# Kernel tuning notes

Hardware: AMD Instinct MI355X
Metric: run time of the kernel (lower is better)

## Reference

```python
import jax, jax.numpy as jnp
import numpy as np

B, T, D, H = 4, 2048, 1024, 16
DH = D // H  # 64


def setup_inputs() -> dict:
    key = jax.random.key(0)
    k1, k2, k3 = jax.random.split(key, 3)
    x = jax.random.normal(k1, (B, T, D), dtype=jnp.float32)
    w_qkv = jax.random.normal(k2, (D, 3 * D), dtype=jnp.float32) * (D ** -0.5)
    w_out = jax.random.normal(k3, (D, D), dtype=jnp.float32) * (D ** -0.5)
    return {"x": x, "w_qkv": w_qkv, "w_out": w_out}


def reference(x, w_qkv, w_out):
    b, t, d = x.shape
    qkv = jnp.einsum('btd,de->bte', x, w_qkv)  # [B,T,3D]
    q, k, v = jnp.split(qkv, 3, axis=-1)
    # [B,H,T,DH]
    q = q.reshape(b, t, H, DH).transpose(0, 2, 1, 3)
    k = k.reshape(b, t, H, DH).transpose(0, 2, 1, 3)
    v = v.reshape(b, t, H, DH).transpose(0, 2, 1, 3)
    logits = jnp.einsum('bhqd,bhkd->bhqk', q, k) * (1.0 / jnp.sqrt(jnp.float32(DH)))
    # causal bias: -inf strictly above the diagonal (key index > query index)
    causal = jnp.tril(jnp.ones((t, t), dtype=bool))
    logits = jnp.where(causal, logits, jnp.float32(-jnp.inf))
    scores = jax.nn.softmax(logits, axis=-1)
    y = jnp.einsum('bhqk,bhkd->bhqd', scores, v)
    y = y.transpose(0, 2, 1, 3).reshape(b, t, d)
    return jnp.einsum('btd,de->bte', y, w_out)
```

## Files before the change

kernel.cpp:

```cpp
#include <hip/hip_runtime.h>
#include <hip/hip_bf16.h>


namespace {
constexpr int kB = 4, kT = 2048, kD = 1024, kH = 16;
constexpr int kM = kB * kT;
constexpr int kNq = 3 * kD;
constexpr float kS = 0.180336880f;
}

typedef unsigned short u16;
typedef short bf16x8 __attribute__((ext_vector_type(8)));
typedef float f32x4 __attribute__((ext_vector_type(4)));

__device__ __forceinline__ u16 f2bf(float f) {
  unsigned int u = __float_as_uint(f);
  u += 0x7fffu + ((u >> 16) & 1u);
  return (u16)(u >> 16);
}
__device__ __forceinline__ unsigned int pack2(float a, float b) {
  return (unsigned int)f2bf(a) | ((unsigned int)f2bf(b) << 16);
}
__device__ __forceinline__ unsigned int cvtpk(float a, float b) {
  unsigned int r;
  asm("v_cvt_pk_bf16_f32 %0, %1, %2" : "=v"(r) : "v"(a), "v"(b));
  return r;
}

__device__ __forceinline__ void gload16(const u16* g, u16* l) {
  __builtin_amdgcn_global_load_lds(
      (const __attribute__((address_space(1))) unsigned int*)(uintptr_t)g,
      (__attribute__((address_space(3))) unsigned int*)(uintptr_t)l, 16, 0, 0);
}

__global__ __launch_bounds__(256) void cvt_bf16(const float* __restrict__ x,
                                                u16* __restrict__ xb) {
  const size_t i = ((size_t)blockIdx.x * 256 + threadIdx.x) * 8;
  const float4 v0 = *(const float4*)(x + i);
  const float4 v1 = *(const float4*)(x + i + 4);
  uint4 p;
  p.x = pack2(v0.x, v0.y);
  p.y = pack2(v0.z, v0.w);
  p.z = pack2(v1.x, v1.y);
  p.w = pack2(v1.z, v1.w);
  *(uint4*)(xb + i) = p;
}

__global__ __launch_bounds__(256) void transpose_bf(const float* __restrict__ W,
                                                    u16* __restrict__ WT,
                                                    int K, int N, int nscale) {
  __shared__ float T[32][33];
  const int tid = threadIdx.x;
  const int nb = blockIdx.x * 32, kb = blockIdx.y * 32;
  const int r = tid >> 3, c = (tid & 7) * 4;
  const float4 v = *(const float4*)&W[(size_t)(kb + r) * N + nb + c];
  T[r][c + 0] = v.x;
  T[r][c + 1] = v.y;
  T[r][c + 2] = v.z;
  T[r][c + 3] = v.w;
  __syncthreads();
  const float s = (nb + r < nscale) ? kS : 1.0f;
  uint2 p;
  p.x = pack2(T[c + 0][r] * s, T[c + 1][r] * s);
  p.y = pack2(T[c + 2][r] * s, T[c + 3][r] * s);
  *(uint2*)&WT[(size_t)(nb + r) * K + kb + c] = p;
}

template <bool F32OUT>
__global__ __launch_bounds__(512, 2) void gemm_mt(const u16* __restrict__ A,
                                                  const u16* __restrict__ BT,
                                                  void* __restrict__ Cv,
                                                  int lda, int ldc) {
  __shared__ u16 As[2][256 * 64];
  __shared__ u16 Bs[2][128 * 64];
  constexpr int NT = kD / 64;
  const int tid = threadIdx.x;
  const int wid = tid >> 6, lane = tid & 63;
  const int col = lane & 15, quad = lane >> 4;
  const int wm_ = wid >> 2, wn_ = wid & 3;

  const int nwg = gridDim.x * gridDim.y;
  int flat = blockIdx.y * gridDim.x + blockIdx.x;
  flat = (flat & 7) * (nwg >> 3) + (flat >> 3);
  const int n0 = (flat % gridDim.x) * 128;
  const int m0 = (flat / gridDim.x) * 256;

  const int srow = tid >> 3;
  const int scol8 = (tid & 7) * 8;
  const int gch8 = ((tid & 7) ^ (srow & 7)) * 8;
  const u16* const Ag = A + (size_t)(m0 + srow) * lda + gch8;
  const u16* const Bg = BT + (size_t)(n0 + srow) * kD + gch8;

  f32x4 acc[8][2];
#pragma unroll
  for (int i = 0; i < 8; ++i)
#pragma unroll
    for (int j = 0; j < 2; ++j) acc[i][j] = (f32x4){0.f, 0.f, 0.f, 0.f};

#define STAGE_AH(buf, half, k0)                                      \
  do {                                                               \
    gload16(Ag + (size_t)((half)*128) * lda + (k0),                  \
            &As[buf][((half)*128 + srow) * 64 + scol8]);             \
    gload16(Ag + (size_t)((half)*128 + 64) * lda + (k0),             \
            &As[buf][((half)*128 + 64 + srow) * 64 + scol8]);        \
  } while (0)
#define STAGE_BF(buf, k0)                                            \
  do {                                                               \
    gload16(Bg + (size_t)(k0), &Bs[buf][srow * 64 + scol8]);         \
    gload16(Bg + (size_t)64 * kD + (k0),                             \
            &Bs[buf][(64 + srow) * 64 + scol8]);                     \
  } while (0)

  STAGE_AH(0, 0, 0);
  STAGE_BF(0, 0);
  STAGE_AH(0, 1, 0);
  STAGE_AH(1, 0, 64);
  STAGE_BF(1, 64);
  asm volatile("s_waitcnt vmcnt(4)" ::: "memory");
  __builtin_amdgcn_s_barrier();

  for (int t = 0; t < NT; ++t) {
    const int cur = t & 1;
    const u16* Ac = &As[cur][0];
    const u16* Bc = &Bs[cur][0];
    bf16x8 af[4][2], bv[2][2];

#pragma unroll
    for (int mi = 0; mi < 4; ++mi) {
      const int r = wm_ * 64 + mi * 16 + col;
#pragma unroll
      for (int ks = 0; ks < 2; ++ks)
        af[mi][ks] =
            *(const bf16x8*)&Ac[r * 64 + (((ks * 4 + quad) ^ (r & 7)) * 8)];
    }
#pragma unroll
    for (int ni = 0; ni < 2; ++ni) {
      const int r = wn_ * 32 + ni * 16 + col;
#pragma unroll
      for (int ks = 0; ks < 2; ++ks)
        bv[ni][ks] =
            *(const bf16x8*)&Bc[r * 64 + (((ks * 4 + quad) ^ (r & 7)) * 8)];
    }
    if (t + 1 < NT) STAGE_AH(cur ^ 1, 1, (t + 1) * 64);
    __builtin_amdgcn_s_barrier();
    asm volatile("s_waitcnt lgkmcnt(0)" ::: "memory");
    __builtin_amdgcn_s_setprio(1);
#pragma unroll
    for (int mi = 0; mi < 4; ++mi)
#pragma unroll
      for (int ni = 0; ni < 2; ++ni)
#pragma unroll
        for (int ks = 0; ks < 2; ++ks)
          acc[mi][ni] = __builtin_amdgcn_mfma_f32_16x16x32_bf16(
              af[mi][ks], bv[ni][ks], acc[mi][ni], 0, 0, 0);
    __builtin_amdgcn_s_setprio(0);
    if (t + 1 < NT)
      asm volatile("s_waitcnt vmcnt(6)" ::: "memory");
    else
      asm volatile("s_waitcnt vmcnt(0)" ::: "memory");
    __builtin_amdgcn_s_barrier();

#pragma unroll
    for (int mi = 0; mi < 4; ++mi) {
      const int r = 128 + wm_ * 64 + mi * 16 + col;
#pragma unroll
      for (int ks = 0; ks < 2; ++ks)
        af[mi][ks] =
            *(const bf16x8*)&Ac[r * 64 + (((ks * 4 + quad) ^ (r & 7)) * 8)];
    }
    if (t + 2 < NT) {
      STAGE_AH(cur, 0, (t + 2) * 64);
      STAGE_BF(cur, (t + 2) * 64);
    }
    __builtin_amdgcn_s_barrier();
    asm volatile("s_waitcnt lgkmcnt(0)" ::: "memory");
    __builtin_amdgcn_s_setprio(1);
#pragma unroll
    for (int mi = 0; mi < 4; ++mi)
#pragma unroll
      for (int ni = 0; ni < 2; ++ni)
#pragma unroll
        for (int ks = 0; ks < 2; ++ks)
          acc[4 + mi][ni] = __builtin_amdgcn_mfma_f32_16x16x32_bf16(
              af[mi][ks], bv[ni][ks], acc[4 + mi][ni], 0, 0, 0);
    __builtin_amdgcn_s_setprio(0);
    if (t + 2 < NT)
      asm volatile("s_waitcnt vmcnt(6)" ::: "memory");
    else if (t + 1 < NT)
      asm volatile("s_waitcnt vmcnt(2)" ::: "memory");
    __builtin_amdgcn_s_barrier();
  }
#undef STAGE_AH
#undef STAGE_BF

#pragma unroll
  for (int mh = 0; mh < 2; ++mh)
#pragma unroll
    for (int mi = 0; mi < 4; ++mi) {
      const int row = m0 + mh * 128 + wm_ * 64 + mi * 16 + quad * 4;
#pragma unroll
      for (int reg = 0; reg < 4; ++reg) {
#pragma unroll
        for (int ni = 0; ni < 2; ++ni) {
          const int cc = n0 + wn_ * 32 + ni * 16 + col;
          if (F32OUT)
            ((float*)Cv)[(size_t)(row + reg) * ldc + cc] =
                acc[mh * 4 + mi][ni][reg];
          else
            ((u16*)Cv)[(size_t)(row + reg) * ldc + cc] =
                f2bf(acc[mh * 4 + mi][ni][reg]);
        }
      }
    }
}

__global__ __launch_bounds__(256) void attn_fwd(u16* __restrict__ qkv) {
  __shared__ u16 Ks[2][64 * 64];
  __shared__ u16 Vt[64][68];
  __shared__ u16 Ps[64][68];
  const int tid = threadIdx.x;
  const int w = tid >> 6, lane = tid & 63;
  const int col = lane & 15, quad = lane >> 4;
  const int bh = blockIdx.x;
  const int b = bh >> 4, h = bh & 15;
  const int pa = blockIdx.y;
  const size_t base = (size_t)(b * kT) * kNq + h * 64;

  const int krr = lane >> 3;
  const int ksw = (lane & 7) ^ krr;
  const u16* const kgbase =
      qkv + base + kD + (size_t)(w * 16 + krr) * kNq + ksw * 8;

  const int vkp = (tid & 31) * 2, vd0 = (tid >> 5) * 8;
  const u16* const vgbase = qkv + base + 2 * kD + (size_t)vkp * kNq + vd0;

  bf16x8 onesf;
#pragma unroll
  for (int i = 0; i < 8; ++i) onesf[i] = (short)0x3F80;

  int cur = 0;
#pragma unroll
  for (int pass = 0; pass < 2; ++pass) {
    const int qt = pass ? (31 - pa) : pa;
    const int q0 = qt << 6;

    bf16x8 aq[2];
#pragma unroll
    for (int ks = 0; ks < 2; ++ks)
      aq[ks] = *(const bf16x8*)(qkv + base + (size_t)(q0 + w * 16 + col) * kNq +
                                ks * 32 + quad * 8);

    gload16(kgbase, &Ks[cur][(w * 16) * 64]);
    gload16(kgbase + (size_t)8 * kNq, &Ks[cur][(w * 16 + 8) * 64]);
    uint4 va = *(const uint4*)vgbase;
    uint4 vb = *(const uint4*)(vgbase + kNq);

    f32x4 o[4];
#pragma unroll
    for (int nt = 0; nt < 4; ++nt) o[nt] = (f32x4){0.f, 0.f, 0.f, 0.f};
    f32x4 o4 = (f32x4){0.f, 0.f, 0.f, 0.f};

    for (int kt = 0; kt <= qt; ++kt) {
      __syncthreads();
      {
        const unsigned int* aw = (const unsigned int*)&va;
        const unsigned int* bw = (const unsigned int*)&vb;
#pragma unroll
        for (int i = 0; i < 4; ++i) {
          *(unsigned int*)&Vt[vd0 + 2 * i][vkp] =
              __builtin_amdgcn_perm(bw[i], aw[i], 0x05040100u);
          *(unsigned int*)&Vt[vd0 + 2 * i + 1][vkp] =
              __builtin_amdgcn_perm(bw[i], aw[i], 0x07060302u);
        }
      }
      __syncthreads();

      if (kt < qt) {
        const size_t ko = (size_t)((kt + 1) << 6) * kNq;
        gload16(kgbase + ko, &Ks[cur ^ 1][(w * 16) * 64]);
        gload16(kgbase + ko + (size_t)8 * kNq, &Ks[cur ^ 1][(w * 16 + 8) * 64]);
        va = *(const uint4*)(vgbase + ko);
        vb = *(const uint4*)(vgbase + ko + kNq);
      }

      f32x4 st[4];
#pragma unroll
      for (int nt = 0; nt < 4; ++nt) st[nt] = (f32x4){0.f, 0.f, 0.f, 0.f};
#pragma unroll
      for (int ks = 0; ks < 2; ++ks) {
#pragma unroll
        for (int nt = 0; nt < 4; ++nt) {
          const int kr = nt * 16 + col;
          const bf16x8 bk = *(const bf16x8*)&Ks[cur][kr * 64 +
                                                     (((ks * 4 + quad) ^
                                                       (col & 7)) *
                                                      8)];
          st[nt] = __builtin_amdgcn_mfma_f32_16x16x32_bf16(bk, aq[ks], st[nt],
                                                           0, 0, 0);
        }
      }

      if (kt == qt) {
        const int qrel = w * 16 + col;
#pragma unroll
        for (int nt = 0; nt < 4; ++nt)
#pragma unroll
          for (int reg = 0; reg < 4; ++reg) {
            const int krel = nt * 16 + quad * 4 + reg;
            st[nt][reg] =
                (krel <= qrel) ? __builtin_amdgcn_exp2f(st[nt][reg]) : 0.f;
          }
      } else {
#pragma unroll
        for (int nt = 0; nt < 4; ++nt)
#pragma unroll
          for (int reg = 0; reg < 4; ++reg)
            st[nt][reg] = __builtin_amdgcn_exp2f(st[nt][reg]);
      }

#pragma unroll
      for (int nt = 0; nt < 4; ++nt) {
        uint2 pk;
        pk.x = cvtpk(st[nt][0], st[nt][1]);
        pk.y = cvtpk(st[nt][2], st[nt][3]);
        *(uint2*)&Ps[w * 16 + col][nt * 16 + quad * 4] = pk;
      }

#pragma unroll
      for (int ks = 0; ks < 2; ++ks) {
        const bf16x8 ap =
            *(const bf16x8*)&Ps[w * 16 + col][ks * 32 + quad * 8];
#pragma unroll
        for (int nt = 0; nt < 4; ++nt) {
          const bf16x8 bv =
              *(const bf16x8*)&Vt[nt * 16 + col][ks * 32 + quad * 8];
          o[nt] = __builtin_amdgcn_mfma_f32_16x16x32_bf16(ap, bv, o[nt], 0, 0,
                                                          0);
        }
        o4 = __builtin_amdgcn_mfma_f32_16x16x32_bf16(ap, onesf, o4, 0, 0, 0);
      }
      cur ^= 1;
    }

#pragma unroll
    for (int reg = 0; reg < 4; ++reg) {
      const float inv = 1.0f / o4[reg];
      u16* yp = qkv + base + (size_t)(q0 + w * 16 + quad * 4 + reg) * kNq;
#pragma unroll
      for (int nt = 0; nt < 4; ++nt)
        yp[nt * 16 + col] = f2bf(o[nt][reg] * inv);
    }
  }
}

extern "C" void kernel_launch(void* const* d_in, const int* in_sizes, int n_in,
                              void* d_out, int out_size, void* d_ws,
                              size_t ws_size, hipStream_t stream) {
  const float* x = (const float*)d_in[0];
  const float* w_qkv = (const float*)d_in[1];
  const float* w_out = (const float*)d_in[2];

  u16* wqkvT = (u16*)d_ws;
  u16* woutT = wqkvT + (size_t)kNq * kD;
  u16* qkvb = woutT + (size_t)kD * kD;
  u16* xb = (u16*)d_out;

  cvt_bf16<<<kM * kD / 2048, 256, 0, stream>>>(x, xb);
  transpose_bf<<<dim3(kNq / 32, kD / 32), 256, 0, stream>>>(w_qkv, wqkvT, kD,
                                                            kNq, kD);
  transpose_bf<<<dim3(kD / 32, kD / 32), 256, 0, stream>>>(w_out, woutT, kD,
                                                           kD, 0);
  gemm_mt<false><<<dim3(kNq / 128, kM / 256), 512, 0, stream>>>(xb, wqkvT,
                                                                qkvb, kD, kNq);
  attn_fwd<<<dim3(kB * kH, 16), 256, 0, stream>>>(qkvb);
  gemm_mt<true><<<dim3(kD / 128, kM / 256), 512, 0, stream>>>(qkvb, woutT,
                                                              d_out, kNq, kD);
}
```

Before: 249.0 us.

## Use 256x256 tiled GEMM with ping-pong half-tile staging for QKV projection

```diff
diff --git a/kernel.cpp b/kernel.cpp
--- a/kernel.cpp
+++ b/kernel.cpp
@@ -67,6 +67,155 @@
 }
 
 template <bool F32OUT>
+__global__ __launch_bounds__(512, 2) void gemm256b(const u16* __restrict__ A,
+                                                   const u16* __restrict__ BT,
+                                                   void* __restrict__ Cv,
+                                                   int lda, int ldc) {
+  __shared__ u16 As[2][256 * 64];
+  __shared__ u16 Bs[2][256 * 64];
+  constexpr int NT = kD / 64;
+  const int tid = threadIdx.x;
+  const int wid = tid >> 6, lane = tid & 63;
+  const int col = lane & 15, quad = lane >> 4;
+  const int wm_ = wid >> 2, wn_ = wid & 3;
+
+  const int nwg = gridDim.x * gridDim.y;
+  int flat = blockIdx.y * gridDim.x + blockIdx.x;
+  flat = (flat & 7) * (nwg >> 3) + (flat >> 3);
+  const int n0 = (flat % gridDim.x) * 256;
+  const int m0 = (flat / gridDim.x) * 256;
+
+  const int srow = tid >> 3;
+  const int scol8 = (tid & 7) * 8;
+  const int gch8 = ((tid & 7) ^ (srow & 7)) * 8;
+  const u16* const Ag = A + (size_t)(m0 + srow) * lda + gch8;
+  const u16* const Bg = BT + (size_t)(n0 + srow) * kD + gch8;
+
+  f32x4 acc[8][4];
+#pragma unroll
+  for (int i = 0; i < 8; ++i)
+#pragma unroll
+    for (int j = 0; j < 4; ++j) acc[i][j] = (f32x4){0.f, 0.f, 0.f, 0.f};
+
+#define STAGE_AH(buf, half, k0)                                      \
+  do {                                                               \
+    gload16(Ag + (size_t)((half)*128) * lda + (k0),                  \
+            &As[buf][((half)*128 + srow) * 64 + scol8]);             \
+    gload16(Ag + (size_t)((half)*128 + 64) * lda + (k0),             \
+            &As[buf][((half)*128 + 64 + srow) * 64 + scol8]);        \
+  } while (0)
+#define STAGE_BH(buf, half, k0)                                      \
+  do {                                                               \
+    gload16(Bg + (size_t)((half)*128) * kD + (k0),                   \
+            &Bs[buf][((half)*128 + srow) * 64 + scol8]);             \
+    gload16(Bg + (size_t)((half)*128 + 64) * kD + (k0),              \
+            &Bs[buf][((half)*128 + 64 + srow) * 64 + scol8]);        \
+  } while (0)
+
+  STAGE_AH(0, 0, 0);
+  STAGE_BH(0, 0, 0);
+  STAGE_BH(0, 1, 0);
+  STAGE_AH(0, 1, 0);
+  asm volatile("s_waitcnt vmcnt(2)" ::: "memory");
+  __builtin_amdgcn_s_barrier();
+
+  for (int t = 0; t < NT; ++t) {
+    const int cur = t & 1, nxt = cur ^ 1;
+    const u16* Ac = &As[cur][0];
+    const u16* Bc = &Bs[cur][0];
+    const int k1 = (t + 1) * 64;
+    const bool pf = (t + 1 < NT);
+    bf16x8 af[4], bv[4];
+
+#define READ_A(KS, MH)                                                        \
+  do {                                                                        \
+    _Pragma("unroll") for (int mi = 0; mi < 4; ++mi) {                        \
+      const int r = (MH)*128 + wm_ * 64 + mi * 16 + col;                      \
+      af[mi] =                                                                \
+          *(const bf16x8*)&Ac[r * 64 + ((((KS)*4 + quad) ^ (r & 7)) * 8)];    \
+    }                                                                         \
+  } while (0)
+#define READ_B(KS)                                                            \
+  do {                                                                        \
+    _Pragma("unroll") for (int ni = 0; ni < 4; ++ni) {                        \
+      const int r = wn_ * 64 + ni * 16 + col;                                 \
+      bv[ni] =                                                                \
+          *(const bf16x8*)&Bc[r * 64 + ((((KS)*4 + quad) ^ (r & 7)) * 8)];    \
+    }                                                                         \
+  } while (0)
+#define MFMA16(MH)                                                            \
+  do {                                                                        \
+    __builtin_amdgcn_s_setprio(1);                                            \
+    _Pragma("unroll") for (int mi = 0; mi < 4; ++mi)                          \
+        _Pragma("unroll") for (int ni = 0; ni < 4; ++ni) acc[(MH)*4 + mi][ni] \
+        = __builtin_amdgcn_mfma_f32_16x16x32_bf16(af[mi], bv[ni],             \
+                                                  acc[(MH)*4 + mi][ni], 0, 0, \
+                                                  0);                         \
+    __builtin_amdgcn_s_setprio(0);                                            \
+  } while (0)
+
+    READ_A(0, 0);
+    READ_B(0);
+    if (pf) STAGE_AH(nxt, 0, k1);
+    __builtin_amdgcn_s_barrier();
+    asm volatile("s_waitcnt lgkmcnt(0)" ::: "memory");
+    MFMA16(0);
+    if (pf)
+      asm volatile("s_waitcnt vmcnt(2)" ::: "memory");
+    else
+      asm volatile("s_waitcnt vmcnt(0)" ::: "memory");
+    __builtin_amdgcn_s_barrier();
+
+    READ_A(0, 1);
+    if (pf) STAGE_BH(nxt, 0, k1);
+    __builtin_amdgcn_s_barrier();
+    asm volatile("s_waitcnt lgkmcnt(0)" ::: "memory");
+    MFMA16(1);
+    __builtin_amdgcn_s_barrier();
+
+    READ_A(1, 0);
+    READ_B(1);
+    if (pf) STAGE_BH(nxt, 1, k1);
+    __builtin_amdgcn_s_barrier();
+    asm volatile("s_waitcnt lgkmcnt(0)" ::: "memory");
+    MFMA16(0);
+    __builtin_amdgcn_s_barrier();
+
+    READ_A(1, 1);
+    if (pf) STAGE_AH(nxt, 1, k1);
+    __builtin_amdgcn_s_barrier();
+    asm volatile("s_waitcnt lgkmcnt(0)" ::: "memory");
+    MFMA16(1);
+    if (pf)
+      asm volatile("s_waitcnt vmcnt(2)" ::: "memory");
+    __builtin_amdgcn_s_barrier();
+
+#undef READ_A
+#undef READ_B
+#undef MFMA16
+  }
+#undef STAGE_AH
+#undef STAGE_BH
+
+#pragma unroll
+  for (int mig = 0; mig < 8; ++mig) {
+    const int row =
+        m0 + (mig >> 2) * 128 + wm_ * 64 + (mig & 3) * 16 + quad * 4;
+#pragma unroll
+    for (int reg = 0; reg < 4; ++reg) {
+#pragma unroll
+      for (int nig = 0; nig < 4; ++nig) {
+        const int cc = n0 + wn_ * 64 + nig * 16 + col;
+        if (F32OUT)
+          ((float*)Cv)[(size_t)(row + reg) * ldc + cc] = acc[mig][nig][reg];
+        else
+          ((u16*)Cv)[(size_t)(row + reg) * ldc + cc] = f2bf(acc[mig][nig][reg]);
+      }
+    }
+  }
+}
+
+template <bool F32OUT>
 __global__ __launch_bounds__(512, 2) void gemm_mt(const u16* __restrict__ A,
                                                   const u16* __restrict__ BT,
                                                   void* __restrict__ Cv,
@@ -370,8 +519,9 @@
                                                             kNq, kD);
   transpose_bf<<<dim3(kD / 32, kD / 32), 256, 0, stream>>>(w_out, woutT, kD,
                                                            kD, 0);
-  gemm_mt<false><<<dim3(kNq / 128, kM / 256), 512, 0, stream>>>(xb, wqkvT,
-                                                                qkvb, kD, kNq);
+  gemm256b<false><<<dim3(kNq / 256, kM / 256), 512, 0, stream>>>(xb, wqkvT,
+                                                                 qkvb, kD,
+                                                                 kNq);
   attn_fwd<<<dim3(kB * kH, 16), 256, 0, stream>>>(qkvb);
   gemm_mt<true><<<dim3(kD / 128, kM / 256), 512, 0, stream>>>(qkvb, woutT,
                                                               d_out, kNq, kD);
```

Measured after the change: 249.6 us. No clear change (+0.2%).
